# Kernel tuning notes

Hardware: AMD Instinct MI355X
Metric: run time of the kernel (lower is better)

Reference implementation:

```python
import jax, jax.numpy as jnp
import numpy as np

N_FINE = 50000
N_COARSE = 25000
N_EDGES = 800000
DIM = 128


def setup_inputs() -> dict:
    key = jax.random.key(0)
    k1, k2, k3, k4, k5 = jax.random.split(key, 5)
    feat = jax.random.normal(k1, (N_COARSE, DIM), dtype=jnp.float32)
    src = jax.random.randint(k2, (N_EDGES,), 0, N_FINE, dtype=jnp.int32)
    dst = jax.random.randint(k3, (N_EDGES,), 0, N_FINE, dtype=jnp.int32)
    # select_idx must be unique fine-graph ids (scatter-set semantics)
    select_idx = jax.random.permutation(k4, N_FINE)[:N_COARSE].astype(jnp.int32)
    # GraphConv params (glorot-ish init)
    weight = jax.random.normal(k5, (DIM, DIM), dtype=jnp.float32) / np.sqrt(DIM)
    bias = jnp.zeros((DIM,), dtype=jnp.float32)
    return {"feat": feat, "src": src, "dst": dst, "select_idx": select_idx,
            "weight": weight, "bias": bias, "num_nodes": N_FINE}


def reference(feat, src, dst, select_idx, weight, bias, num_nodes):
    # 1) Unpool: scatter coarse features into zero fine-graph tensor
    d = feat.shape[-1]
    fine = jnp.zeros((num_nodes, d), dtype=feat.dtype).at[select_idx].set(feat)
    # (dropout is identity in eval mode)
    # 2) GraphConv, norm='both': D_dst^{-1/2} A D_src^{-1/2} X W + b
    ones_e = jnp.ones_like(src, dtype=feat.dtype)
    deg_out = jnp.clip(jax.ops.segment_sum(ones_e, src, num_segments=num_nodes), 1.0)
    deg_in = jnp.clip(jax.ops.segment_sum(ones_e, dst, num_segments=num_nodes), 1.0)
    h = fine * (deg_out ** -0.5)[:, None]          # [N, d] source-side norm
    h = h @ weight                                  # in_feats == out_feats -> mm first
    agg = jax.ops.segment_sum(h[src], dst, num_segments=num_nodes)  # SpMM
    out = agg * (deg_in ** -0.5)[:, None] + bias
    return out
```

## Files before the change

kernel.cpp:

```cpp
#include <hip/hip_runtime.h>

#define DIM 128
#define NBC 128
#define SP 6252

typedef __attribute__((ext_vector_type(8))) short bf16x8;
typedef __attribute__((ext_vector_type(4))) float f32x4;

static __device__ inline short f2bf(float f) {
    union { float f; unsigned u; } x;
    x.f = f;
    unsigned r = (x.u + 0x7FFF + ((x.u >> 16) & 1)) >> 16;
    return (short)r;
}
static __device__ inline float bflo(unsigned u) {
    union { unsigned u; float f; } x; x.u = u << 16; return x.f;
}
static __device__ inline float bfhi(unsigned u) {
    union { unsigned u; float f; } x; x.u = u & 0xFFFF0000u; return x.f;
}

__global__ __launch_bounds__(512) void k_hist(
    const int* __restrict__ src, const int* __restrict__ dst,
    unsigned* __restrict__ partial, int n_edges, int nhalf, int chunk) {
    __shared__ unsigned hist[SP];
    int b = blockIdx.x & (NBC - 1);
    int h = (blockIdx.x >> 7) & 1;
    int cls = blockIdx.x >> 8;
    const int* __restrict__ idx = cls ? dst : src;
    int lo = h * nhalf;

    for (int i = threadIdx.x * 4; i < SP; i += 512 * 4)
        *(uint4*)&hist[i] = make_uint4(0, 0, 0, 0);
    __syncthreads();

    int e0 = b * chunk;
    int e1 = min(e0 + chunk, n_edges);
    int qs = e0 >> 2, qe = e1 >> 2;
#define CNT(x)                                                                     \
    {                                                                              \
        unsigned t = (unsigned)((x) - lo);                                         \
        if (t < (unsigned)nhalf) atomicAdd(&hist[t >> 2], 1u << ((t & 3) * 8));    \
    }
    for (int q = qs + threadIdx.x; q < qe; q += 512) {
        int4 v = ((const int4*)idx)[q];
        CNT(v.x); CNT(v.y); CNT(v.z); CNT(v.w);
    }
    for (int e = (qe << 2) + threadIdx.x; e < e1; e += 512) CNT(idx[e]);
#undef CNT
    __syncthreads();

    unsigned* dp = partial + (size_t)((cls * 2 + h) * NBC + b) * SP;
    for (int i = threadIdx.x * 4; i < SP; i += 512 * 4)
        *(uint4*)&dp[i] = *(const uint4*)&hist[i];
}

__global__ __launch_bounds__(256) void k_hreduce(
    unsigned* __restrict__ partial, float* __restrict__ rso,
    int* __restrict__ deg, float* __restrict__ ri, int* __restrict__ map,
    int* __restrict__ off0, int* __restrict__ blksum,
    int nhalf, int nbh, int n_fine, int n_coarse) {
    int g = blockIdx.x;
    int cls = g / (2 * nbh);
    int rem = g - cls * (2 * nbh);
    int h = rem / nbh;
    int blk = rem - h * nbh;
    int hw = nhalf / 4;
    int w = blk * 256 + threadIdx.x;
    bool valid = (w < hw);

    if (cls == 0) {
        if (!valid) return;
        unsigned s = 0;
        const unsigned* p = partial + (size_t)(h * NBC) * SP + w;
#pragma unroll 8
        for (int b = 0; b < NBC; ++b) s += p[(size_t)b * SP];
        int i0 = h * nhalf + 4 * w;
        int dd[4] = {(int)(s & 255), (int)((s >> 8) & 255), (int)((s >> 16) & 255), (int)(s >> 24)};
        for (int k = 0; k < 4 && i0 + k < n_fine; ++k)
            rso[i0 + k] = rsqrtf((float)max(dd[k], 1));
        return;
    }

    __shared__ int sL[256];
    unsigned run = 0;
    if (valid) {
        unsigned* p = partial + (size_t)((2 + h) * NBC) * SP + w;
#pragma unroll 8
        for (int b = 0; b < NBC; ++b) {
            unsigned* q = p + (size_t)b * SP;
            unsigned t = *q;
            *q = run;
            run += t;
        }
    }
    int d0 = run & 255, d1 = (run >> 8) & 255, d2 = (run >> 16) & 255, d3 = run >> 24;
    int mysum = valid ? (d0 + d1 + d2 + d3) : 0;
    int t = threadIdx.x;
    sL[t] = mysum;
    __syncthreads();
    for (int dd = 1; dd < 256; dd <<= 1) {
        int x = (t >= dd) ? sL[t - dd] : 0;
        __syncthreads();
        if (t >= dd) sL[t] += x;
        __syncthreads();
    }
    int excl = sL[t] - mysum;
    if (t == 255) blksum[h * nbh + blk] = sL[255];
    if (valid) {
        int i0 = h * nhalf + 4 * w;
        int dd[4] = {d0, d1, d2, d3};
        int pf[4] = {excl, excl + d0, excl + d0 + d1, excl + d0 + d1 + d2};
        for (int k = 0; k < 4 && i0 + k < n_fine; ++k) {
            deg[i0 + k] = dd[k];
            ri[i0 + k] = rsqrtf((float)max(dd[k], 1));
            map[i0 + k] = n_coarse;
            off0[i0 + k] = pf[k];
        }
    }
}

__global__ __launch_bounds__(256) void k_gemm(
    const float* __restrict__ feat, const int* __restrict__ sel,
    const float* __restrict__ rso, const float* __restrict__ W,
    unsigned short* __restrict__ hwb, int* __restrict__ map,
    int* __restrict__ blksum, int n_coarse, int nbw) {
    __shared__ short Wl[16384];
    int t = threadIdx.x;

    if (blockIdx.x == 0) {
        if (t < 64) {
            int orig = (t < nbw) ? blksum[t] : 0;
            int v = orig;
#pragma unroll
            for (int dd = 1; dd < 64; dd <<= 1) {
                int x = __shfl_up(v, dd, 64);
                if (t >= dd) v += x;
            }
            if (t < nbw) blksum[t] = v - orig;
        }
        if (t < DIM) hwb[(size_t)n_coarse * DIM + t] = 0;
    }
    for (int gi = blockIdx.x * 256 + t; gi < n_coarse; gi += gridDim.x * 256)
        map[sel[gi]] = gi;

    for (int g = t; g < 2048; g += 256) {
        int n = g & 127;
        int kk = g >> 7;
        int kbase = ((kk >> 2) * 32) + ((kk & 3) * 8);
        bf16x8 v;
#pragma unroll
        for (int j = 0; j < 8; ++j) v[j] = f2bf(W[(size_t)(kbase + j) * DIM + n]);
        *(bf16x8*)&Wl[g * 8] = v;
    }
    __syncthreads();

    int wv = t >> 6, lane = t & 63;
    int lg = lane >> 4;
    int lm = lane & 15;
    int ntiles = (n_coarse + 15) / 16;
    for (int tile = blockIdx.x * 4 + wv; tile < ntiles; tile += gridDim.x * 4) {
        int r0 = tile * 16;
        int ra = min(r0 + lm, n_coarse - 1);
        const float* fr = feat + (size_t)ra * DIM;
        bf16x8 a[4];
#pragma unroll
        for (int kc = 0; kc < 4; ++kc) {
            float4 x0 = *(const float4*)(fr + kc * 32 + lg * 8);
            float4 x1 = *(const float4*)(fr + kc * 32 + lg * 8 + 4);
            bf16x8 av;
            av[0] = f2bf(x0.x); av[1] = f2bf(x0.y); av[2] = f2bf(x0.z); av[3] = f2bf(x0.w);
            av[4] = f2bf(x1.x); av[5] = f2bf(x1.y); av[6] = f2bf(x1.z); av[7] = f2bf(x1.w);
            a[kc] = av;
        }
        f32x4 acc[8];
#pragma unroll
        for (int cb = 0; cb < 8; ++cb) acc[cb] = (f32x4){0.f, 0.f, 0.f, 0.f};
#pragma unroll
        for (int kc = 0; kc < 4; ++kc) {
#pragma unroll
            for (int cb = 0; cb < 8; ++cb) {
                bf16x8 b = *(const bf16x8*)&Wl[(((kc * 4 + lg) * 128) + cb * 16 + lm) * 8];
                acc[cb] = __builtin_amdgcn_mfma_f32_16x16x32_bf16(a[kc], b, acc[cb], 0, 0, 0);
            }
        }
#pragma unroll
        for (int j = 0; j < 4; ++j) {
            int r = r0 + lg * 4 + j;
            if (r < n_coarse) {
                float sc = rso[sel[r]];
                unsigned short* hr = hwb + (size_t)r * DIM + lm;
#pragma unroll
                for (int cb = 0; cb < 8; ++cb)
                    hr[cb * 16] = (unsigned short)f2bf(acc[cb][j] * sc);
            }
        }
    }
}

__global__ __launch_bounds__(512) void k_bucket(
    const int* __restrict__ src, const int* __restrict__ dst, const int* __restrict__ map,
    const int* __restrict__ off0, const int* __restrict__ blksum,
    const unsigned* __restrict__ partial,
    int* __restrict__ bucket, int n_edges, int nhalf, int nbh, int chunk) {
    __shared__ unsigned cur[3125];
    int b = blockIdx.x & (NBC - 1);
    int q = blockIdx.x >> 7;
    int h = q >> 1;
    int qw = nhalf / 8;
    int qrange = nhalf / 2;
    const unsigned* pfx = partial + (size_t)((2 + h) * NBC + b) * SP + (q & 1) * qw;
    for (int i = threadIdx.x; i < qw; i += 512) cur[i] = pfx[i];
    __syncthreads();

    int lo = q * qrange;
    int e0 = b * chunk;
    int e1 = min(e0 + chunk, n_edges);
    int qs = e0 >> 2, qe = e1 >> 2;
#define PROC(d, s)                                                                 \
    {                                                                              \
        unsigned t = (unsigned)((d) - lo);                                         \
        if (t < (unsigned)qrange) {                                                \
            int sh = (t & 3) * 8;                                                  \
            unsigned old = atomicAdd(&cur[t >> 2], 1u << sh);                      \
            int widx = h * nbh + (((d) - h * nhalf) >> 10);                        \
            bucket[off0[d] + blksum[widx] + (int)((old >> sh) & 255)] = map[s];    \
        }                                                                          \
    }
    for (int qq = qs + threadIdx.x; qq < qe; qq += 512) {
        int4 d4 = ((const int4*)dst)[qq];
        int4 s4 = ((const int4*)src)[qq];
        PROC(d4.x, s4.x); PROC(d4.y, s4.y); PROC(d4.z, s4.z); PROC(d4.w, s4.w);
    }
    for (int e = (qe << 2) + threadIdx.x; e < e1; e += 512) PROC(dst[e], src[e]);
#undef PROC
}

__global__ __launch_bounds__(256) void k_gather(
    const int* __restrict__ off0, const int* __restrict__ blksum,
    const int* __restrict__ deg, const float* __restrict__ ri,
    const int* __restrict__ bucket, const uint4* __restrict__ hwb4,
    const float* __restrict__ bias, float* __restrict__ out,
    int n_fine, int nhalf, int nbh) {
    int gid = blockIdx.x * 256 + threadIdx.x;
    int l = gid & 15;
    int grp = gid >> 4;
    int ngrp = (gridDim.x * 256) >> 4;
    float4 b0 = ((const float4*)bias)[l * 2];
    float4 b1 = ((const float4*)bias)[l * 2 + 1];
    for (int v = grp; v < n_fine; v += ngrp) {
        int hh = (v >= nhalf) ? 1 : 0;
        int widx = hh * nbh + ((v - hh * nhalf) >> 10);
        int o = off0[v] + blksum[widx];
        int n = deg[v];
        float a0 = 0, a1 = 0, a2 = 0, a3 = 0, a4 = 0, a5 = 0, a6 = 0, a7 = 0;
        float c0 = 0, c1 = 0, c2 = 0, c3 = 0, c4 = 0, c5 = 0, c6 = 0, c7 = 0;
        int j = 0;
        for (; j + 2 <= n; j += 2) {
            int i0 = __builtin_nontemporal_load(bucket + o + j);
            int i1 = __builtin_nontemporal_load(bucket + o + j + 1);
            uint4 u0 = hwb4[(size_t)i0 * 16 + l];
            uint4 u1 = hwb4[(size_t)i1 * 16 + l];
            a0 += bflo(u0.x); a1 += bfhi(u0.x); a2 += bflo(u0.y); a3 += bfhi(u0.y);
            a4 += bflo(u0.z); a5 += bfhi(u0.z); a6 += bflo(u0.w); a7 += bfhi(u0.w);
            c0 += bflo(u1.x); c1 += bfhi(u1.x); c2 += bflo(u1.y); c3 += bfhi(u1.y);
            c4 += bflo(u1.z); c5 += bfhi(u1.z); c6 += bflo(u1.w); c7 += bfhi(u1.w);
        }
        if (j < n) {
            int i0 = __builtin_nontemporal_load(bucket + o + j);
            uint4 u0 = hwb4[(size_t)i0 * 16 + l];
            a0 += bflo(u0.x); a1 += bfhi(u0.x); a2 += bflo(u0.y); a3 += bfhi(u0.y);
            a4 += bflo(u0.z); a5 += bfhi(u0.z); a6 += bflo(u0.w); a7 += bfhi(u0.w);
        }
        float s = ri[v];
        f32x4 r0, r1;
        r0.x = (a0 + c0) * s + b0.x; r0.y = (a1 + c1) * s + b0.y;
        r0.z = (a2 + c2) * s + b0.z; r0.w = (a3 + c3) * s + b0.w;
        r1.x = (a4 + c4) * s + b1.x; r1.y = (a5 + c5) * s + b1.y;
        r1.z = (a6 + c6) * s + b1.z; r1.w = (a7 + c7) * s + b1.w;
        __builtin_nontemporal_store(r0, (f32x4*)(out + (size_t)v * DIM + l * 8));
        __builtin_nontemporal_store(r1, (f32x4*)(out + (size_t)v * DIM + l * 8 + 4));
    }
}

extern "C" void kernel_launch(void* const* d_in, const int* in_sizes, int n_in,
                              void* d_out, int out_size, void* d_ws, size_t ws_size,
                              hipStream_t stream) {
    const float* feat = (const float*)d_in[0];
    const int* src = (const int*)d_in[1];
    const int* dst = (const int*)d_in[2];
    const int* sel = (const int*)d_in[3];
    const float* W = (const float*)d_in[4];
    const float* bias = (const float*)d_in[5];
    float* out = (float*)d_out;

    int n_fine = out_size / DIM;
    int n_coarse = in_sizes[0] / DIM;
    int n_edges = in_sizes[1];

    int nhalf = ((n_fine / 2) + 3) & ~3;
    int nbh = (nhalf / 4 + 255) / 256;
    int nbw = 2 * nbh;
    int chunk = ((n_edges + NBC - 1) / NBC + 3) & ~3;

    int* map = (int*)d_ws;
    int* off0 = map + n_fine;
    int* deg = off0 + n_fine;
    float* ri = (float*)(deg + n_fine);
    float* rso = ri + n_fine;
    int* blksum = (int*)(rso + n_fine);
    unsigned short* hwb = (unsigned short*)(blksum + 64);
    int* bucket = (int*)(hwb + (size_t)(n_coarse + 1) * DIM);
    unsigned* partial = (unsigned*)(bucket + n_edges);

    int ntiles = (n_coarse + 15) / 16;

    hipLaunchKernelGGL(k_hist, dim3(4 * NBC), dim3(512), 0, stream,
                       src, dst, partial, n_edges, nhalf, chunk);
    hipLaunchKernelGGL(k_hreduce, dim3(4 * nbh), dim3(256), 0, stream,
                       partial, rso, deg, ri, map, off0, blksum, nhalf, nbh, n_fine, n_coarse);
    hipLaunchKernelGGL(k_gemm, dim3((ntiles + 3) / 4), dim3(256), 0, stream,
                       feat, sel, rso, W, hwb, map, blksum, n_coarse, nbw);
    hipLaunchKernelGGL(k_bucket, dim3(4 * NBC), dim3(512), 0, stream,
                       src, dst, map, off0, blksum, partial, bucket, n_edges, nhalf, nbh, chunk);
    hipLaunchKernelGGL(k_gather, dim3((n_fine * 16 + 255) / 256), dim3(256), 0, stream,
                       off0, blksum, deg, ri, bucket, (const uint4*)hwb, bias, out,
                       n_fine, nhalf, nbh);
}
```

Baseline: 80.44 us.

## Run GEMM and bucket-fill concurrently in one kernel; unroll gather by four

Result: no change. 80.89 us (+0.6%).

```diff
diff --git a/kernel.cpp b/kernel.cpp
--- a/kernel.cpp
+++ b/kernel.cpp
@@ -3,6 +3,7 @@
 #define DIM 128
 #define NBC 128
 #define SP 6252
+#define NBKT 512
 
 typedef __attribute__((ext_vector_type(8))) short bf16x8;
 typedef __attribute__((ext_vector_type(4))) float f32x4;
@@ -120,14 +121,10 @@
     }
 }
 
-__global__ __launch_bounds__(256) void k_gemm(
-    const float* __restrict__ feat, const int* __restrict__ sel,
-    const float* __restrict__ rso, const float* __restrict__ W,
-    unsigned short* __restrict__ hwb, int* __restrict__ map,
-    int* __restrict__ blksum, int n_coarse, int nbw) {
-    __shared__ short Wl[16384];
+__global__ __launch_bounds__(256) void k_prep(
+    const int* __restrict__ sel, int* __restrict__ map, int* __restrict__ blksum,
+    unsigned short* __restrict__ hwb, int n_coarse, int nbw) {
     int t = threadIdx.x;
-
     if (blockIdx.x == 0) {
         if (t < 64) {
             int orig = (t < nbw) ? blksum[t] : 0;
@@ -138,20 +135,74 @@
                 if (t >= dd) v += x;
             }
             if (t < nbw) blksum[t] = v - orig;
-        }
-        if (t < DIM) hwb[(size_t)n_coarse * DIM + t] = 0;
-    }
-    for (int gi = blockIdx.x * 256 + t; gi < n_coarse; gi += gridDim.x * 256)
-        map[sel[gi]] = gi;
-
-    for (int g = t; g < 2048; g += 256) {
+        } else if (t >= 128) {
+            hwb[(size_t)n_coarse * DIM + (t - 128)] = 0;
+        }
+    }
+    int gi = blockIdx.x * 256 + t;
+    if (gi < n_coarse) map[sel[gi]] = gi;
+}
+
+union SMem {
+    short Wl[16384];
+    unsigned cur[3200];
+};
+
+__global__ __launch_bounds__(512) void k_work(
+    const int* __restrict__ src, const int* __restrict__ dst, const int* __restrict__ map,
+    const int* __restrict__ off0, const int* __restrict__ blksum,
+    const unsigned* __restrict__ partial, int* __restrict__ bucket,
+    const float* __restrict__ feat, const int* __restrict__ sel,
+    const float* __restrict__ rso, const float* __restrict__ W,
+    unsigned short* __restrict__ hwb,
+    int n_edges, int nhalf, int nbh, int chunk, int n_coarse) {
+    __shared__ SMem sm;
+    int t = threadIdx.x;
+
+    if (blockIdx.x < NBKT) {
+        int b = blockIdx.x & (NBC - 1);
+        int q = blockIdx.x >> 7;
+        int h = q >> 1;
+        int qw = nhalf / 8;
+        int qrange = nhalf / 2;
+        const unsigned* pfx = partial + (size_t)((2 + h) * NBC + b) * SP + (q & 1) * qw;
+        for (int i = t; i < qw; i += 512) sm.cur[i] = pfx[i];
+        __syncthreads();
+
+        int lo = q * qrange;
+        int e0 = b * chunk;
+        int e1 = min(e0 + chunk, n_edges);
+        int qs = e0 >> 2, qe = e1 >> 2;
+#define PROC(d, s)                                                                 \
+    {                                                                              \
+        unsigned tt = (unsigned)((d) - lo);                                        \
+        if (tt < (unsigned)qrange) {                                               \
+            int sh = (tt & 3) * 8;                                                 \
+            unsigned old = atomicAdd(&sm.cur[tt >> 2], 1u << sh);                  \
+            int widx = h * nbh + (((d) - h * nhalf) >> 10);                        \
+            bucket[off0[d] + blksum[widx] + (int)((old >> sh) & 255)] = map[s];    \
+        }                                                                          \
+    }
+        for (int qq = qs + t; qq < qe; qq += 512) {
+            int4 d4 = ((const int4*)dst)[qq];
+            int4 s4 = ((const int4*)src)[qq];
+            PROC(d4.x, s4.x); PROC(d4.y, s4.y); PROC(d4.z, s4.z); PROC(d4.w, s4.w);
+        }
+        for (int e = (qe << 2) + t; e < e1; e += 512) PROC(dst[e], src[e]);
+#undef PROC
+        return;
+    }
+
+    int gb = blockIdx.x - NBKT;
+    int ngb = gridDim.x - NBKT;
+    for (int g = t; g < 2048; g += 512) {
         int n = g & 127;
         int kk = g >> 7;
         int kbase = ((kk >> 2) * 32) + ((kk & 3) * 8);
         bf16x8 v;
 #pragma unroll
         for (int j = 0; j < 8; ++j) v[j] = f2bf(W[(size_t)(kbase + j) * DIM + n]);
-        *(bf16x8*)&Wl[g * 8] = v;
+        *(bf16x8*)&sm.Wl[g * 8] = v;
     }
     __syncthreads();
 
@@ -159,7 +210,7 @@
     int lg = lane >> 4;
     int lm = lane & 15;
     int ntiles = (n_coarse + 15) / 16;
-    for (int tile = blockIdx.x * 4 + wv; tile < ntiles; tile += gridDim.x * 4) {
+    for (int tile = gb * 8 + wv; tile < ntiles; tile += ngb * 8) {
         int r0 = tile * 16;
         int ra = min(r0 + lm, n_coarse - 1);
         const float* fr = feat + (size_t)ra * DIM;
@@ -180,7 +231,7 @@
         for (int kc = 0; kc < 4; ++kc) {
 #pragma unroll
             for (int cb = 0; cb < 8; ++cb) {
-                bf16x8 b = *(const bf16x8*)&Wl[(((kc * 4 + lg) * 128) + cb * 16 + lm) * 8];
+                bf16x8 b = *(const bf16x8*)&sm.Wl[(((kc * 4 + lg) * 128) + cb * 16 + lm) * 8];
                 acc[cb] = __builtin_amdgcn_mfma_f32_16x16x32_bf16(a[kc], b, acc[cb], 0, 0, 0);
             }
         }
@@ -196,44 +247,6 @@
             }
         }
     }
-}
-
-__global__ __launch_bounds__(512) void k_bucket(
-    const int* __restrict__ src, const int* __restrict__ dst, const int* __restrict__ map,
-    const int* __restrict__ off0, const int* __restrict__ blksum,
-    const unsigned* __restrict__ partial,
-    int* __restrict__ bucket, int n_edges, int nhalf, int nbh, int chunk) {
-    __shared__ unsigned cur[3125];
-    int b = blockIdx.x & (NBC - 1);
-    int q = blockIdx.x >> 7;
-    int h = q >> 1;
-    int qw = nhalf / 8;
-    int qrange = nhalf / 2;
-    const unsigned* pfx = partial + (size_t)((2 + h) * NBC + b) * SP + (q & 1) * qw;
-    for (int i = threadIdx.x; i < qw; i += 512) cur[i] = pfx[i];
-    __syncthreads();
-
-    int lo = q * qrange;
-    int e0 = b * chunk;
-    int e1 = min(e0 + chunk, n_edges);
-    int qs = e0 >> 2, qe = e1 >> 2;
-#define PROC(d, s)                                                                 \
-    {                                                                              \
-        unsigned t = (unsigned)((d) - lo);                                         \
-        if (t < (unsigned)qrange) {                                                \
-            int sh = (t & 3) * 8;                                                  \
-            unsigned old = atomicAdd(&cur[t >> 2], 1u << sh);                      \
-            int widx = h * nbh + (((d) - h * nhalf) >> 10);                        \
-            bucket[off0[d] + blksum[widx] + (int)((old >> sh) & 255)] = map[s];    \
-        }                                                                          \
-    }
-    for (int qq = qs + threadIdx.x; qq < qe; qq += 512) {
-        int4 d4 = ((const int4*)dst)[qq];
-        int4 s4 = ((const int4*)src)[qq];
-        PROC(d4.x, s4.x); PROC(d4.y, s4.y); PROC(d4.z, s4.z); PROC(d4.w, s4.w);
-    }
-    for (int e = (qe << 2) + threadIdx.x; e < e1; e += 512) PROC(dst[e], src[e]);
-#undef PROC
 }
 
 __global__ __launch_bounds__(256) void k_gather(
@@ -256,17 +269,25 @@
         float a0 = 0, a1 = 0, a2 = 0, a3 = 0, a4 = 0, a5 = 0, a6 = 0, a7 = 0;
         float c0 = 0, c1 = 0, c2 = 0, c3 = 0, c4 = 0, c5 = 0, c6 = 0, c7 = 0;
         int j = 0;
-        for (; j + 2 <= n; j += 2) {
+        for (; j + 4 <= n; j += 4) {
             int i0 = __builtin_nontemporal_load(bucket + o + j);
             int i1 = __builtin_nontemporal_load(bucket + o + j + 1);
+            int i2 = __builtin_nontemporal_load(bucket + o + j + 2);
+            int i3 = __builtin_nontemporal_load(bucket + o + j + 3);
             uint4 u0 = hwb4[(size_t)i0 * 16 + l];
             uint4 u1 = hwb4[(size_t)i1 * 16 + l];
+            uint4 u2 = hwb4[(size_t)i2 * 16 + l];
+            uint4 u3 = hwb4[(size_t)i3 * 16 + l];
             a0 += bflo(u0.x); a1 += bfhi(u0.x); a2 += bflo(u0.y); a3 += bfhi(u0.y);
             a4 += bflo(u0.z); a5 += bfhi(u0.z); a6 += bflo(u0.w); a7 += bfhi(u0.w);
             c0 += bflo(u1.x); c1 += bfhi(u1.x); c2 += bflo(u1.y); c3 += bfhi(u1.y);
             c4 += bflo(u1.z); c5 += bfhi(u1.z); c6 += bflo(u1.w); c7 += bfhi(u1.w);
-        }
-        if (j < n) {
+            a0 += bflo(u2.x); a1 += bfhi(u2.x); a2 += bflo(u2.y); a3 += bfhi(u2.y);
+            a4 += bflo(u2.z); a5 += bfhi(u2.z); a6 += bflo(u2.w); a7 += bfhi(u2.w);
+            c0 += bflo(u3.x); c1 += bfhi(u3.x); c2 += bflo(u3.y); c3 += bfhi(u3.y);
+            c4 += bflo(u3.z); c5 += bfhi(u3.z); c6 += bflo(u3.w); c7 += bfhi(u3.w);
+        }
+        for (; j < n; ++j) {
             int i0 = __builtin_nontemporal_load(bucket + o + j);
             uint4 u0 = hwb4[(size_t)i0 * 16 + l];
             a0 += bflo(u0.x); a1 += bfhi(u0.x); a2 += bflo(u0.y); a3 += bfhi(u0.y);
@@ -314,15 +335,17 @@
     unsigned* partial = (unsigned*)(bucket + n_edges);
 
     int ntiles = (n_coarse + 15) / 16;
+    int ngb = (ntiles + 7) / 8;
 
     hipLaunchKernelGGL(k_hist, dim3(4 * NBC), dim3(512), 0, stream,
                        src, dst, partial, n_edges, nhalf, chunk);
     hipLaunchKernelGGL(k_hreduce, dim3(4 * nbh), dim3(256), 0, stream,
                        partial, rso, deg, ri, map, off0, blksum, nhalf, nbh, n_fine, n_coarse);
-    hipLaunchKernelGGL(k_gemm, dim3((ntiles + 3) / 4), dim3(256), 0, stream,
-                       feat, sel, rso, W, hwb, map, blksum, n_coarse, nbw);
-    hipLaunchKernelGGL(k_bucket, dim3(4 * NBC), dim3(512), 0, stream,
-                       src, dst, map, off0, blksum, partial, bucket, n_edges, nhalf, nbh, chunk);
+    hipLaunchKernelGGL(k_prep, dim3((n_coarse + 255) / 256), dim3(256), 0, stream,
+                       sel, map, blksum, hwb, n_coarse, nbw);
+    hipLaunchKernelGGL(k_work, dim3(NBKT + ngb), dim3(512), 0, stream,
+                       src, dst, map, off0, blksum, partial, bucket,
+                       feat, sel, rso, W, hwb, n_edges, nhalf, nbh, chunk, n_coarse);
     hipLaunchKernelGGL(k_gather, dim3((n_fine * 16 + 255) / 256), dim3(256), 0, stream,
                        off0, blksum, deg, ri, bucket, (const uint4*)hwb, bias, out,
                        n_fine, nhalf, nbh);
```
